# Kernel tuning notes

Hardware: AMD Instinct MI355X
Metric: run time of the kernel (lower is better)

Reference implementation:

```python
import jax, jax.numpy as jnp
import numpy as np

T = 4096
I = 512    # input_size
H = 2048   # hidden_layer_size
O = 1      # output_size

def setup_inputs() -> dict:
    key = jax.random.key(0)
    ks = jax.random.split(key, 7)
    s_ih = 1.0 / np.sqrt(H)
    return {
        "input_seq": jax.random.normal(ks[0], (T, I), dtype=jnp.float32),
        "W_ih": jax.random.uniform(ks[1], (4 * H, I), minval=-s_ih, maxval=s_ih, dtype=jnp.float32),
        "W_hh": jax.random.uniform(ks[2], (4 * H, H), minval=-s_ih, maxval=s_ih, dtype=jnp.float32),
        "b_ih": jax.random.uniform(ks[3], (4 * H,), minval=-s_ih, maxval=s_ih, dtype=jnp.float32),
        "b_hh": jax.random.uniform(ks[4], (4 * H,), minval=-s_ih, maxval=s_ih, dtype=jnp.float32),
        "W_lin": jax.random.uniform(ks[5], (O, H), minval=-s_ih, maxval=s_ih, dtype=jnp.float32),
        "b_lin": jax.random.uniform(ks[6], (O,), minval=-s_ih, maxval=s_ih, dtype=jnp.float32),
    }

def _lstm_last_h(x, W_ih, W_hh, b_ih, b_hh):
    # Precompute input contributions for all timesteps: [T, 4H]
    x_gates = x @ W_ih.T + (b_ih + b_hh)
    h0 = jnp.zeros((H,), dtype=x.dtype)
    c0 = jnp.zeros((H,), dtype=x.dtype)

    def step(carry, xg):
        h, c = carry
        gates = xg + h @ W_hh.T  # [4H]
        i, f, g, o = jnp.split(gates, 4)  # PyTorch gate order: i, f, g, o
        i = jax.nn.sigmoid(i)
        f = jax.nn.sigmoid(f)
        g = jnp.tanh(g)
        o = jax.nn.sigmoid(o)
        c = f * c + i * g
        h = o * jnp.tanh(c)
        return (h, c), None

    (h_T, _), _ = jax.lax.scan(step, (h0, c0), x_gates)
    return h_T

def reference(input_seq, W_ih, W_hh, b_ih, b_hh, W_lin, b_lin):
    # Module returns predictions[-1] = linear(lstm_out[-1]); only last h is needed.
    h_T = _lstm_last_h(input_seq, W_ih, W_hh, b_ih, b_hh)
    return h_T @ W_lin.T + b_lin  # shape [O]
```

## Files before the change

kernel.cpp:

```cpp
#include <hip/hip_runtime.h>


#define T_STEPS 4096
#define HID     2048
#define GATES   8192
#define KIN     512
#define NWG     256
#define NTHR    512
#define NREP    4
#define XG_BYTES ((size_t)T_STEPS * GATES * 4)
#define HCOM_BYTES ((size_t)NREP * 2 * HID * 8)

typedef float v2f __attribute__((ext_vector_type(2)));

__device__ __forceinline__ float u2f(unsigned int u) {
    union { unsigned int u; float f; } x; x.u = u; return x.f;
}
__device__ __forceinline__ float fast_sigmoid(float x) {
    return 1.f / (1.f + __expf(-x));
}
__device__ __forceinline__ float fast_tanh(float x) {
    return 2.f / (1.f + __expf(-2.f * x)) - 1.f;
}

__global__ __launch_bounds__(256) void gemm_xg(const float* __restrict__ A,
                                               const float* __restrict__ B,
                                               const float* __restrict__ bih,
                                               const float* __restrict__ bhh,
                                               float* __restrict__ C) {
    __shared__ float As[32][68];
    __shared__ float Bs[32][68];
    const int t  = threadIdx.x;
    const int tx = t & 15, ty = t >> 4;
    const int m0 = blockIdx.y * 64, n0 = blockIdx.x * 64;
    const int sr = t >> 3, sc = (t & 7) * 4;

    float c[4][4] = {};
    for (int k0 = 0; k0 < KIN; k0 += 32) {
        float4 a0 = *(const float4*)(A + (size_t)(m0 + sr)      * KIN + k0 + sc);
        float4 a1 = *(const float4*)(A + (size_t)(m0 + sr + 32) * KIN + k0 + sc);
        float4 b0 = *(const float4*)(B + (size_t)(n0 + sr)      * KIN + k0 + sc);
        float4 b1 = *(const float4*)(B + (size_t)(n0 + sr + 32) * KIN + k0 + sc);
        __syncthreads();
        As[sc+0][sr] = a0.x; As[sc+1][sr] = a0.y; As[sc+2][sr] = a0.z; As[sc+3][sr] = a0.w;
        As[sc+0][sr+32] = a1.x; As[sc+1][sr+32] = a1.y; As[sc+2][sr+32] = a1.z; As[sc+3][sr+32] = a1.w;
        Bs[sc+0][sr] = b0.x; Bs[sc+1][sr] = b0.y; Bs[sc+2][sr] = b0.z; Bs[sc+3][sr] = b0.w;
        Bs[sc+0][sr+32] = b1.x; Bs[sc+1][sr+32] = b1.y; Bs[sc+2][sr+32] = b1.z; Bs[sc+3][sr+32] = b1.w;
        __syncthreads();
#pragma unroll
        for (int kk = 0; kk < 32; ++kk) {
            float4 av = *(const float4*)&As[kk][ty * 4];
            float4 bv = *(const float4*)&Bs[kk][tx * 4];
            c[0][0] = fmaf(av.x, bv.x, c[0][0]); c[0][1] = fmaf(av.x, bv.y, c[0][1]);
            c[0][2] = fmaf(av.x, bv.z, c[0][2]); c[0][3] = fmaf(av.x, bv.w, c[0][3]);
            c[1][0] = fmaf(av.y, bv.x, c[1][0]); c[1][1] = fmaf(av.y, bv.y, c[1][1]);
            c[1][2] = fmaf(av.y, bv.z, c[1][2]); c[1][3] = fmaf(av.y, bv.w, c[1][3]);
            c[2][0] = fmaf(av.z, bv.x, c[2][0]); c[2][1] = fmaf(av.z, bv.y, c[2][1]);
            c[2][2] = fmaf(av.z, bv.z, c[2][2]); c[2][3] = fmaf(av.z, bv.w, c[2][3]);
            c[3][0] = fmaf(av.w, bv.x, c[3][0]); c[3][1] = fmaf(av.w, bv.y, c[3][1]);
            c[3][2] = fmaf(av.w, bv.z, c[3][2]); c[3][3] = fmaf(av.w, bv.w, c[3][3]);
        }
    }
    const int col = n0 + tx * 4;
    float4 bias;
    bias.x = bih[col]   + bhh[col];
    bias.y = bih[col+1] + bhh[col+1];
    bias.z = bih[col+2] + bhh[col+2];
    bias.w = bih[col+3] + bhh[col+3];
    const int bb = (col >> 3) & (NWG - 1);
    const int gg = col >> 11;
    const int uu = col & 7;
    float* dst = C + (size_t)bb * T_STEPS * 32 + gg * 8 + uu;
#pragma unroll
    for (int i = 0; i < 4; ++i) {
        float4 o;
        o.x = c[i][0] + bias.x; o.y = c[i][1] + bias.y;
        o.z = c[i][2] + bias.z; o.w = c[i][3] + bias.w;
        *(float4*)(dst + (size_t)(m0 + ty * 4 + i) * 32) = o;
    }
}

template<int USE_XG>
__global__ __launch_bounds__(NTHR, 2) void lstm_rec(
    const float* __restrict__ X,
    const float* __restrict__ Wih,
    const float* __restrict__ xg,
    const float* __restrict__ Whh,
    const float* __restrict__ bih,
    const float* __restrict__ bhh,
    unsigned long long* __restrict__ hcom)
{
    const int t  = threadIdx.x;
    const int kc = t & 127;
    const int rg = t >> 7;
    const int j0 = blockIdx.x * 8;
    const int rep = blockIdx.x & (NREP - 1);

    v2f whh2[8][8];
#pragma unroll
    for (int m = 0; m < 8; ++m) {
        const float* wr = Whh + (size_t)(rg * HID + j0 + m) * HID + kc;
#pragma unroll
        for (int j = 0; j < 8; ++j) {
            v2f p; p.x = wr[(2 * j) * 128]; p.y = wr[(2 * j + 1) * 128];
            whh2[m][j] = p;
        }
    }
    float wih[8][4];
    if (!USE_XG) {
#pragma unroll
        for (int m = 0; m < 8; ++m) {
            float4 vx = *(const float4*)(Wih + (size_t)(rg * HID + j0 + m) * KIN + kc * 4);
            wih[m][0] = vx.x; wih[m][1] = vx.y; wih[m][2] = vx.z; wih[m][3] = vx.w;
        }
    }

    float brow = 0.f;
    if (t < 32) {
        const int grow = (t >> 3) * HID + j0 + (t & 7);
        brow = bih[grow] + bhh[grow];
    }

    __shared__ float hshare[HID];
    __shared__ float comb[64];
    float c_state = 0.f;

    for (int s = 0; s < T_STEPS; ++s) {
        float xgv = 0.f;
        if (USE_XG && t < 32)
            xgv = xg[((size_t)blockIdx.x * T_STEPS + s) * 32 + t];

        v2f hv2[8];
        if (t < 128) {
            if (t >= 64 && s > 0) __builtin_amdgcn_s_sleep(8);
            const unsigned long long* hp = hcom + ((size_t)rep * 2 + (s & 1)) * HID;
            unsigned long long v[16];
            int guard = 1 << 18;
            for (;;) {
#pragma unroll
                for (int g = 0; g < 16; ++g)
                    v[g] = __hip_atomic_load(hp + g * 128 + kc, __ATOMIC_RELAXED,
                                             __HIP_MEMORY_SCOPE_AGENT);
                bool ok = true;
#pragma unroll
                for (int g = 0; g < 16; ++g)
                    ok &= ((unsigned int)v[g] >= (unsigned int)s);
                if (ok || --guard <= 0) break;
                __builtin_amdgcn_s_sleep(1);
            }
#pragma unroll
            for (int j = 0; j < 8; ++j) {
                v2f p;
                p.x = u2f((unsigned int)(v[2 * j] >> 32));
                p.y = u2f((unsigned int)(v[2 * j + 1] >> 32));
                hv2[j] = p;
                hshare[(2 * j) * 128 + kc]     = p.x;
                hshare[(2 * j + 1) * 128 + kc] = p.y;
            }
        }
        __syncthreads();
        if (t >= 128) {
#pragma unroll
            for (int j = 0; j < 8; ++j) {
                v2f p;
                p.x = hshare[(2 * j) * 128 + kc];
                p.y = hshare[(2 * j + 1) * 128 + kc];
                hv2[j] = p;
            }
        }

        v2f acc2[8];
        if (!USE_XG) {
            float4 x4 = *(const float4*)(X + (size_t)s * KIN + kc * 4);
#pragma unroll
            for (int m = 0; m < 8; ++m) {
                float a = wih[m][0] * x4.x;
                a = fmaf(wih[m][1], x4.y, a);
                a = fmaf(wih[m][2], x4.z, a);
                a = fmaf(wih[m][3], x4.w, a);
                v2f z; z.x = a; z.y = 0.f; acc2[m] = z;
            }
        } else {
#pragma unroll
            for (int m = 0; m < 8; ++m) { v2f z; z.x = 0.f; z.y = 0.f; acc2[m] = z; }
        }

#pragma unroll
        for (int m = 0; m < 8; ++m) {
            v2f a = acc2[m];
#pragma unroll
            for (int j = 0; j < 8; ++j)
                a = __builtin_elementwise_fma(whh2[m][j], hv2[j], a);
            acc2[m] = a;
        }

        float sm[8];
#pragma unroll
        for (int m = 0; m < 8; ++m) sm[m] = acc2[m].x + acc2[m].y;
#pragma unroll
        for (int m = 0; m < 8; ++m) {
            sm[m] += __shfl_xor(sm[m], 1, 64);
            sm[m] += __shfl_xor(sm[m], 2, 64);
            sm[m] += __shfl_xor(sm[m], 4, 64);
        }
        {
            const int l  = t & 63;
            const int r7 = l & 7;
            float p = sm[0];
            p = (r7 == 1) ? sm[1] : p;
            p = (r7 == 2) ? sm[2] : p;
            p = (r7 == 3) ? sm[3] : p;
            p = (r7 == 4) ? sm[4] : p;
            p = (r7 == 5) ? sm[5] : p;
            p = (r7 == 6) ? sm[6] : p;
            p = (r7 == 7) ? sm[7] : p;
            p += __shfl_xor(p, 8, 64);
            p += __shfl_xor(p, 16, 64);
            p += __shfl_xor(p, 32, 64);
            if (l < 8)
                comb[(t >> 7) * 16 + ((t >> 6) & 1) * 8 + l] = p;
        }
        __syncthreads();

        if (t < 32) {
            const int ci = (t >> 3) * 16 + (t & 7);
            float sum = comb[ci] + comb[ci + 8] + brow + xgv;
            const float a1 = __shfl_down(sum, 8, 64);
            const float a2 = __shfl_down(sum, 16, 64);
            const float a3 = __shfl_down(sum, 24, 64);
            if (t < 8) {
                const float i_s = fast_sigmoid(sum);
                const float f_s = fast_sigmoid(a1);
                const float g_t = fast_tanh(a2);
                const float o_s = fast_sigmoid(a3);
                c_state = f_s * c_state + i_s * g_t;
                const float h = o_s * fast_tanh(c_state);
                const unsigned long long pk =
                    ((unsigned long long)__float_as_uint(h) << 32) | (unsigned int)(s + 1);
                const size_t slot = (size_t)((s + 1) & 1) * HID + j0 + t;
#pragma unroll
                for (int r = 0; r < NREP; ++r)
                    __hip_atomic_store(&hcom[(size_t)r * 2 * HID + slot], pk,
                                       __ATOMIC_RELAXED, __HIP_MEMORY_SCOPE_AGENT);
            }
        }
    }
}

__global__ __launch_bounds__(256) void final_linear(const unsigned long long* __restrict__ hcom,
                                                    const float* __restrict__ Wlin,
                                                    const float* __restrict__ blin,
                                                    float* __restrict__ out) {
    __shared__ float red[4];
    const int t = threadIdx.x;
    float a = 0.f;
#pragma unroll
    for (int e = 0; e < 8; ++e) {
        const int idx = t * 8 + e;
        a = fmaf(Wlin[idx], u2f((unsigned int)(hcom[idx] >> 32)), a);
    }
#pragma unroll
    for (int m = 1; m < 64; m <<= 1) a += __shfl_xor(a, m, 64);
    if ((t & 63) == 0) red[t >> 6] = a;
    __syncthreads();
    if (t == 0) out[0] = red[0] + red[1] + red[2] + red[3] + blin[0];
}

extern "C" void kernel_launch(void* const* d_in, const int* in_sizes, int n_in,
                              void* d_out, int out_size, void* d_ws, size_t ws_size,
                              hipStream_t stream) {
    const float* X    = (const float*)d_in[0];
    const float* Wih  = (const float*)d_in[1];
    const float* Whh  = (const float*)d_in[2];
    const float* bih  = (const float*)d_in[3];
    const float* bhh  = (const float*)d_in[4];
    const float* Wlin = (const float*)d_in[5];
    const float* blin = (const float*)d_in[6];
    float* out = (float*)d_out;

    char* ws = (char*)d_ws;
    const bool big = ws_size >= XG_BYTES + HCOM_BYTES;

    if (big) {
        float* xg = (float*)ws;
        unsigned long long* hcom = (unsigned long long*)(ws + XG_BYTES);
        (void)hipMemsetAsync(hcom, 0, HCOM_BYTES, stream);
        gemm_xg<<<dim3(GATES / 64, T_STEPS / 64), 256, 0, stream>>>(X, Wih, bih, bhh, xg);
        lstm_rec<1><<<dim3(NWG), dim3(NTHR), 0, stream>>>(X, Wih, xg, Whh, bih, bhh, hcom);
        final_linear<<<1, 256, 0, stream>>>(hcom, Wlin, blin, out);
    } else {
        unsigned long long* hcom = (unsigned long long*)ws;
        (void)hipMemsetAsync(hcom, 0, HCOM_BYTES, stream);
        lstm_rec<0><<<dim3(NWG), dim3(NTHR), 0, stream>>>(X, Wih, nullptr, Whh, bih, bhh, hcom);
        final_linear<<<1, 256, 0, stream>>>(hcom, Wlin, blin, out);
    }
}
```

Baseline: 11.17 ms.

## Poll h directly in all threads and spread replica stores across a wavefront

Every thread now polls the global h-communication buffer itself, replacing the 128-thread poll plus LDS broadcast and one __syncthreads per step. The replica count rises from 4 to 8 so more pollers share the load. The 8 h values are shuffled across 64 lanes, so each replica store is issued in parallel instead of looping serially. This removes a block barrier and LDS round trip from the recurrent critical path, but multiplies global polling traffic across all 512 threads per workgroup and could contend on L2.

```diff
diff --git a/kernel.cpp b/kernel.cpp
--- a/kernel.cpp
+++ b/kernel.cpp
@@ -7,7 +7,7 @@
 #define KIN     512
 #define NWG     256
 #define NTHR    512
-#define NREP    4
+#define NREP    8
 #define XG_BYTES ((size_t)T_STEPS * GATES * 4)
 #define HCOM_BYTES ((size_t)NREP * 2 * HID * 8)
 
@@ -121,7 +121,6 @@
         brow = bih[grow] + bhh[grow];
     }
 
-    __shared__ float hshare[HID];
     __shared__ float comb[64];
     float c_state = 0.f;
 
@@ -130,11 +129,10 @@
         if (USE_XG && t < 32)
             xgv = xg[((size_t)blockIdx.x * T_STEPS + s) * 32 + t];
 
-        v2f hv2[8];
-        if (t < 128) {
-            if (t >= 64 && s > 0) __builtin_amdgcn_s_sleep(8);
-            const unsigned long long* hp = hcom + ((size_t)rep * 2 + (s & 1)) * HID;
-            unsigned long long v[16];
+        if (t >= 64 && s > 0) __builtin_amdgcn_s_sleep(8);
+        const unsigned long long* hp = hcom + ((size_t)rep * 2 + (s & 1)) * HID;
+        unsigned long long v[16];
+        {
             int guard = 1 << 18;
             for (;;) {
 #pragma unroll
@@ -148,25 +146,14 @@
                 if (ok || --guard <= 0) break;
                 __builtin_amdgcn_s_sleep(1);
             }
-#pragma unroll
-            for (int j = 0; j < 8; ++j) {
-                v2f p;
-                p.x = u2f((unsigned int)(v[2 * j] >> 32));
-                p.y = u2f((unsigned int)(v[2 * j + 1] >> 32));
-                hv2[j] = p;
-                hshare[(2 * j) * 128 + kc]     = p.x;
-                hshare[(2 * j + 1) * 128 + kc] = p.y;
-            }
-        }
-        __syncthreads();
-        if (t >= 128) {
-#pragma unroll
-            for (int j = 0; j < 8; ++j) {
-                v2f p;
-                p.x = hshare[(2 * j) * 128 + kc];
-                p.y = hshare[(2 * j + 1) * 128 + kc];
-                hv2[j] = p;
-            }
+        }
+        v2f hv2[8];
+#pragma unroll
+        for (int j = 0; j < 8; ++j) {
+            v2f p;
+            p.x = u2f((unsigned int)(v[2 * j] >> 32));
+            p.y = u2f((unsigned int)(v[2 * j + 1] >> 32));
+            hv2[j] = p;
         }
 
         v2f acc2[8];
@@ -222,27 +209,30 @@
         }
         __syncthreads();
 
-        if (t < 32) {
-            const int ci = (t >> 3) * 16 + (t & 7);
-            float sum = comb[ci] + comb[ci + 8] + brow + xgv;
+        if (t < 64) {
+            float sum = 0.f;
+            if (t < 32) {
+                const int ci = (t >> 3) * 16 + (t & 7);
+                sum = comb[ci] + comb[ci + 8] + brow + xgv;
+            }
             const float a1 = __shfl_down(sum, 8, 64);
             const float a2 = __shfl_down(sum, 16, 64);
             const float a3 = __shfl_down(sum, 24, 64);
+            float h_val = 0.f;
             if (t < 8) {
                 const float i_s = fast_sigmoid(sum);
                 const float f_s = fast_sigmoid(a1);
                 const float g_t = fast_tanh(a2);
                 const float o_s = fast_sigmoid(a3);
                 c_state = f_s * c_state + i_s * g_t;
-                const float h = o_s * fast_tanh(c_state);
-                const unsigned long long pk =
-                    ((unsigned long long)__float_as_uint(h) << 32) | (unsigned int)(s + 1);
-                const size_t slot = (size_t)((s + 1) & 1) * HID + j0 + t;
-#pragma unroll
-                for (int r = 0; r < NREP; ++r)
-                    __hip_atomic_store(&hcom[(size_t)r * 2 * HID + slot], pk,
-                                       __ATOMIC_RELAXED, __HIP_MEMORY_SCOPE_AGENT);
-            }
+                h_val = o_s * fast_tanh(c_state);
+            }
+            const float hb = __shfl(h_val, t & 7, 64);
+            const unsigned long long pk =
+                ((unsigned long long)__float_as_uint(hb) << 32) | (unsigned int)(s + 1);
+            __hip_atomic_store(hcom + (size_t)(t >> 3) * 2 * HID +
+                                   (size_t)((s + 1) & 1) * HID + j0 + (t & 7),
+                               pk, __ATOMIC_RELAXED, __HIP_MEMORY_SCOPE_AGENT);
         }
     }
 }
```

After: 13.25 ms. +18.6%, slower.
